# Performance work log

Measured on AMD Instinct MI355X. Metric: run time of the kernel, lower is better.

The kernel has to match this reference:

```python
import jax, jax.numpy as jnp
import numpy as np

# Matches the torch constant: 1/sqrt(2*3.14159) (NOT math.pi)
INV_SQRT_2PI = 1.0 / np.sqrt(np.float32(2.0 * 3.14159))


def density_ir_normal(x):
    return INV_SQRT_2PI * jnp.exp(-0.5 * x * x)


def setup_inputs() -> dict:
    key = jax.random.key(0)
    k1, k2, k3 = jax.random.split(key, 3)
    batch = 8388608           # 2**23 output slots
    n_events = 16777216       # 2**24 scattered events (avg 2 per slot)
    idx = jax.random.randint(k1, (n_events,), 0, batch)
    vals = jax.random.normal(k2, (n_events,), dtype=jnp.float32)
    # theta0 in (0,1) (branch prob), theta1 > 0 (scale), theta2 (loc)
    thetas = jnp.array([0.7, 1.3, 0.2], dtype=jnp.float32)
    return {"batch": batch, "idx": idx, "vals": vals, "thetas": thetas}


def reference(batch, idx, vals, thetas):
    # l_4_high = min(thetas[0], 1); l_5 = max(l_4_high, 0) -> clip(theta0, 0, 1)
    l_5_lhs_integral = jnp.clip(thetas[0], 0.0, 1.0)
    l_1_cond = 1.0 - l_5_lhs_integral
    # per-event multiplicative factor (vectorized density evaluation)
    z = (vals - thetas[2]) / thetas[1]
    factors = (1.0 - l_1_cond) * density_ir_normal(z) / thetas[1]
    # multiplicative scatter; duplicate indices multiply in (matches the
    # sequential result[idx[i]] *= factor loop, product is order-invariant)
    result = jnp.ones(batch, dtype=vals.dtype).at[idx].multiply(factors)
    return result * l_1_cond
```

## Files before the change

### kernel.cpp

```cpp
#include <hip/hip_runtime.h>
#include <climits>


#define INV_SQRT_2PI 0.39894246f
#define SLOT_BITS 14
#define SLOTS (1 << SLOT_BITS)
#define NB_MAX 512
#define NBLK 512
#define BTHREADS 1024
#define TILE 4096
#define RING 32
#define QSCALE 8192.0f
#define QMASK 0x3FFFFu
#define CMASK 0xFFFFFu

#define LDS_BAR() do {                                        \
    asm volatile("s_waitcnt lgkmcnt(0)" ::: "memory");        \
    __builtin_amdgcn_s_barrier();                             \
} while (0)

__device__ __forceinline__ long long region_idx(int blk, int b, int nbuckets,
                                                int swzmask) {
    int bb = swzmask ? ((b + blk) & swzmask) : b;
    return (long long)blk * nbuckets + bb;
}

__device__ __forceinline__ void ovf_push(uint2* ovf, int* ovf_cnt, int ovcap,
                                         unsigned gslot, unsigned q) {
    int op = atomicAdd(ovf_cnt, 1);
    if (op < ovcap) ovf[op] = make_uint2(gslot, q);
}

__global__ __launch_bounds__(BTHREADS) void bin_kernel(
        const int* __restrict__ idx, const float* __restrict__ vals,
        const float* __restrict__ thetas,
        unsigned* __restrict__ pairs,
        int* __restrict__ fill,
        uint2* __restrict__ ovf, int* __restrict__ ovf_cnt, int ovcap,
        int n, int nbuckets, int cap_shift, int swzmask, int epb) {
    __shared__ unsigned ring[RING * NB_MAX];
    __shared__ int scnt[NB_MAX];

    const int tid = threadIdx.x;
    const int blk = blockIdx.x;
    const int cappb = 1 << cap_shift;
    long long start = (long long)blk * epb;
    long long end = start + epb;
    if (end > n) end = n;

    for (int b = tid; b < nbuckets; b += BTHREADS) scnt[b] = 0;
    __syncthreads();

    const float t1 = thetas[1], t2 = thetas[2];
    const float t0c = fminf(fmaxf(thetas[0], 0.0f), 1.0f);
    const float inv_t1 = 1.0f / t1;

    int4 ck = make_int4(0,0,0,0); float4 cv = make_float4(0,0,0,0); int ccnt = 0;
    int4 pk_; float4 pv_;
    {
        long long te0 = start + TILE; if (te0 > end) te0 = end;
        long long base = start + (long long)tid * 4;
        if (base + 4 <= te0) {
            ck = *(const int4*)(idx + base);
            cv = *(const float4*)(vals + base);
            ccnt = 4;
        } else if (base < te0) {
            ccnt = (int)(te0 - base);
            int kk[4] = {0,0,0,0}; float vv[4] = {0,0,0,0};
            for (int i = 0; i < ccnt; ++i) { kk[i]=idx[base+i]; vv[i]=vals[base+i]; }
            ck = make_int4(kk[0],kk[1],kk[2],kk[3]);
            cv = make_float4(vv[0],vv[1],vv[2],vv[3]);
        }
    }

    for (long long ts = start; ts < end; ts += TILE) {
        int ncnt = 0;
        long long tsn = ts + TILE;
        if (tsn < end) {
            long long ten = tsn + TILE; if (ten > end) ten = end;
            long long base = tsn + (long long)tid * 4;
            if (base + 4 <= ten) {
                pk_ = *(const int4*)(idx + base);
                pv_ = *(const float4*)(vals + base);
                ncnt = 4;
            } else if (base < ten) {
                ncnt = (int)(ten - base);
                int kk[4] = {0,0,0,0}; float vv[4] = {0,0,0,0};
                for (int i = 0; i < ncnt; ++i) { kk[i]=idx[base+i]; vv[i]=vals[base+i]; }
                pk_ = make_int4(kk[0],kk[1],kk[2],kk[3]);
                pv_ = make_float4(vv[0],vv[1],vv[2],vv[3]);
            }
        }

        int   kk[4] = {ck.x, ck.y, ck.z, ck.w};
        float vv[4] = {cv.x, cv.y, cv.z, cv.w};
        int bs[4]; unsigned recs[4];
        #pragma unroll
        for (int j = 0; j < 4; ++j) {
            unsigned uk = (unsigned)kk[j];
            bs[j] = (int)(uk >> SLOT_BITS);
            float z = (vv[j] - t2) * inv_t1;
            float u = 0.5f * z * z;
            unsigned q = __float2uint_rn(fminf(u * QSCALE, (float)QMASK));
            recs[j] = ((uk & (SLOTS - 1)) << 18) | q;
        }
        int ret[4];
        #pragma unroll
        for (int j = 0; j < 4; ++j) {
            ret[j] = (j < ccnt && bs[j] < nbuckets)
                     ? atomicAdd(&scnt[bs[j]], 1) : INT_MIN;
        }
        #pragma unroll
        for (int j = 0; j < 4; ++j) {
            if (ret[j] == INT_MIN) continue;
            int pos = ret[j] & CMASK;
            int fl  = (ret[j] >> 20) << 4;
            if (pos - fl < RING)
                ring[(pos & (RING - 1)) * nbuckets + bs[j]] = recs[j];
            else
                ovf_push(ovf, ovf_cnt, ovcap, (unsigned)kk[j], recs[j] & QMASK);
        }
        LDS_BAR();

        for (int b = tid; b < nbuckets; b += BTHREADS) {
            int pk = scnt[b];
            int c = pk & CMASK;
            int J = pk >> 20;
            int fl = J << 4;
            int se = c < fl + RING ? c : fl + RING;
            int na = se - fl;
            int J0 = J;
            while (na >= 16) {
                int H = (J & 1) << 4;
                unsigned tmp[16];
                #pragma unroll
                for (int i = 0; i < 16; ++i)
                    tmp[i] = ring[(H + i) * nbuckets + b];
                if (J < (cappb >> 4)) {
                    uint4* d4 = (uint4*)(pairs +
                        (region_idx(blk, b, nbuckets, swzmask) << cap_shift) + (J << 4));
                    const uint4* t4 = (const uint4*)tmp;
                    d4[0]=t4[0]; d4[1]=t4[1]; d4[2]=t4[2]; d4[3]=t4[3];
                } else {
                    for (int i = 0; i < 16; ++i) {
                        unsigned r = tmp[i];
                        ovf_push(ovf, ovf_cnt, ovcap,
                                 ((unsigned)b << SLOT_BITS) | (r >> 18), r & QMASK);
                    }
                }
                ++J; fl += 16; na -= 16;
            }
            if (J != J0 || se != c) scnt[b] = (J << 20) | se;
        }
        LDS_BAR();

        ck = pk_; cv = pv_; ccnt = ncnt;
    }

    for (int b = tid; b < nbuckets; b += BTHREADS) {
        int pk = scnt[b];
        int c = pk & CMASK;
        int J = pk >> 20;
        int fl = J << 4;
        int r = c - fl;
        int valid = fl;
        if (r > 0 && J < (cappb >> 4)) {
            int H = (J & 1) << 4;
            unsigned tmp[16];
            #pragma unroll
            for (int i = 0; i < 16; ++i)
                tmp[i] = ring[(H + i) * nbuckets + b];
            uint4* d4 = (uint4*)(pairs +
                (region_idx(blk, b, nbuckets, swzmask) << cap_shift) + (J << 4));
            const uint4* t4 = (const uint4*)tmp;
            d4[0]=t4[0]; d4[1]=t4[1]; d4[2]=t4[2]; d4[3]=t4[3];
            valid = fl + r;
        } else if (r > 0) {
            int H = (J & 1) << 4;
            for (int i = 0; i < r; ++i) {
                unsigned rr = ring[(H + i) * nbuckets + b];
                ovf_push(ovf, ovf_cnt, ovcap,
                         ((unsigned)b << SLOT_BITS) | (rr >> 18), rr & QMASK);
            }
        }
        fill[region_idx(blk, b, nbuckets, swzmask)] = valid;
    }
}

__global__ __launch_bounds__(1024) void reduce_kernel(
        const unsigned* __restrict__ pairs, const int* __restrict__ fill,
        const uint2* __restrict__ ovf, const int* __restrict__ ovf_cnt, int ovcap,
        const float* __restrict__ thetas, float* __restrict__ out,
        long long n_out, int nbuckets, int cap_shift, int swzmask) {
    __shared__ unsigned accu[SLOTS];
    const int tid = threadIdx.x;
    const int b = blockIdx.x;

    for (int s = tid; s < SLOTS; s += 1024) accu[s] = 0u;
    __syncthreads();

    const int wave = tid >> 6, lane = tid & 63;
    const int SEGS = NBLK / 16;

    int sl = wave + (lane & 31) * 16;
    int cntv = fill[region_idx(sl, b, nbuckets, swzmask)];

    const unsigned* pc = pairs +
        (region_idx(wave, b, nbuckets, swzmask) << cap_shift);
    unsigned a0 = pc[lane];
    unsigned a1 = pc[64 + lane];

    for (int i = 0; i < SEGS; ++i) {
        const unsigned* pn = pc; unsigned n0 = 0, n1 = 0;
        if (i < SEGS - 1) {
            int sn = wave + (i + 1) * 16;
            pn = pairs + (region_idx(sn, b, nbuckets, swzmask) << cap_shift);
            n0 = pn[lane];
            n1 = pn[64 + lane];
        }
        int ca = __builtin_amdgcn_readlane(cntv, i);
        if (lane < ca)      atomicAdd(&accu[a0 >> 18], (1u << 25) + (a0 & QMASK));
        if (64 + lane < ca) atomicAdd(&accu[a1 >> 18], (1u << 25) + (a1 & QMASK));
        for (int r = 128 + lane; r < ca; r += 64) {
            unsigned rec = pc[r];
            atomicAdd(&accu[rec >> 18], (1u << 25) + (rec & QMASK));
        }
        pc = pn; a0 = n0; a1 = n1;
    }
    __syncthreads();

    int no = *ovf_cnt; if (no > ovcap) no = ovcap;
    for (int i = tid; i < no; i += 1024) {
        uint2 e = ovf[i];
        if ((int)(e.x >> SLOT_BITS) == b)
            atomicAdd(&accu[e.x & (SLOTS - 1)], (1u << 25) + e.y);
    }
    __syncthreads();

    const float t1 = thetas[1];
    const float t0c = fminf(fmaxf(thetas[0], 0.0f), 1.0f);
    const float logC = logf(t0c * INV_SQRT_2PI / t1);
    const float cond = 1.0f - t0c;
    long long obase = (long long)b << SLOT_BITS;
    for (int ss = tid; ss < SLOTS; ss += 1024) {
        long long o = obase + ss;
        if (o < n_out) {
            unsigned av = accu[ss];
            float v = (float)(av >> 25) * logC
                    - (float)(av & 0x1FFFFFFu) * (1.0f / QSCALE);
            out[o] = cond * expf(v);
        }
    }
}

__global__ void init_zero_kernel(float* __restrict__ out, int n) {
    int i = blockIdx.x * blockDim.x + threadIdx.x;
    int stride = gridDim.x * blockDim.x;
    for (; i < n; i += stride) out[i] = 0.0f;
}
__global__ void scatter_log_kernel(const int* __restrict__ idx,
                                   const float* __restrict__ vals,
                                   const float* __restrict__ thetas,
                                   float* __restrict__ acc, int n) {
    float t1 = thetas[1], t2 = thetas[2];
    float t0c = fminf(fmaxf(thetas[0], 0.0f), 1.0f);
    float logC = logf(t0c * INV_SQRT_2PI / t1);
    float inv_t1 = 1.0f / t1;
    int i = blockIdx.x * blockDim.x + threadIdx.x;
    int stride = gridDim.x * blockDim.x;
    for (; i < n; i += stride) {
        float z = (vals[i] - t2) * inv_t1;
        atomicAdd(&acc[idx[i]], fmaf(-0.5f * z, z, logC));
    }
}
__global__ void finalize_kernel(float* __restrict__ out,
                                const float* __restrict__ thetas, int n) {
    float t0c = fminf(fmaxf(thetas[0], 0.0f), 1.0f);
    float cond = 1.0f - t0c;
    int i = blockIdx.x * blockDim.x + threadIdx.x;
    int stride = gridDim.x * blockDim.x;
    for (; i < n; i += stride) out[i] = cond * expf(out[i]);
}

extern "C" void kernel_launch(void* const* d_in, const int* in_sizes, int n_in,
                              void* d_out, int out_size, void* d_ws, size_t ws_size,
                              hipStream_t stream) {
    const int*   idx    = (const int*)d_in[1];
    const float* vals   = (const float*)d_in[2];
    const float* thetas = (const float*)d_in[3];
    float*       out    = (float*)d_out;

    int n_events = in_sizes[1];
    long long n_out = out_size;
    int nbuckets = (int)((n_out + SLOTS - 1) >> SLOT_BITS);

    long long tiles_total = ((long long)n_events + TILE - 1) / TILE;
    long long tpb = (tiles_total + NBLK - 1) / NBLK;
    int epb = (int)(tpb * TILE);
    long long avg = nbuckets > 0 ? (epb + nbuckets - 1) / nbuckets : 1;
    long long want = avg + avg / 2 + 32;
    int cap_shift = 6;
    while ((1LL << cap_shift) < want && cap_shift < 20) ++cap_shift;
    long long cappb = 1LL << cap_shift;
    int swzmask = (nbuckets > 0 && (nbuckets & (nbuckets - 1)) == 0)
                  ? nbuckets - 1 : 0;

    size_t pairs_b = (size_t)NBLK * nbuckets * cappb * 4;
    size_t fill_b  = (size_t)NBLK * nbuckets * 4;
    size_t head    = pairs_b + fill_b + 64;
    bool fast = (nbuckets > 0) && (nbuckets <= NB_MAX) && (n_events > 0) &&
                (ws_size >= head + 64 * 1024) &&
                ((long long)NBLK * 2048  , true);

    if (fast) {
        unsigned* pairs = (unsigned*)d_ws;
        int* fill = (int*)((char*)d_ws + pairs_b);
        int* ovf_cnt = (int*)((char*)d_ws + pairs_b + fill_b);
        uint2* ovf = (uint2*)((char*)d_ws + head);
        long long ovcap_ll = (long long)((ws_size - head) / 8);
        int ovcap = (int)(ovcap_ll > 4194304 ? 4194304 : ovcap_ll);

        hipMemsetAsync(ovf_cnt, 0, sizeof(int), stream);
        bin_kernel<<<NBLK, BTHREADS, 0, stream>>>(idx, vals, thetas, pairs, fill,
                                                  ovf, ovf_cnt, ovcap,
                                                  n_events, nbuckets, cap_shift,
                                                  swzmask, epb);
        reduce_kernel<<<nbuckets, 1024, 0, stream>>>(pairs, fill, ovf, ovf_cnt,
                                                     ovcap, thetas, out,
                                                     n_out, nbuckets, cap_shift,
                                                     swzmask);
    } else {
        const int BLOCK = 256;
        int grid_out = min((int)((n_out + BLOCK - 1) / BLOCK), 2048);
        int grid_ev  = min((n_events + BLOCK - 1) / BLOCK, 2048);
        init_zero_kernel<<<grid_out, BLOCK, 0, stream>>>(out, (int)n_out);
        scatter_log_kernel<<<grid_ev, BLOCK, 0, stream>>>(idx, vals, thetas, out, n_events);
        finalize_kernel<<<grid_out, BLOCK, 0, stream>>>(out, thetas, (int)n_out);
    }
}
```

Baseline: 96.43 us.

## Double-buffer bin rings so flushing overlaps binning with one barrier per tile

```diff
diff --git a/kernel.cpp b/kernel.cpp
--- a/kernel.cpp
+++ b/kernel.cpp
@@ -3,15 +3,15 @@
 
 
 #define INV_SQRT_2PI 0.39894246f
-#define SLOT_BITS 14
+#define SLOT_BITS 15
 #define SLOTS (1 << SLOT_BITS)
-#define NB_MAX 512
+#define NB 256
 #define NBLK 512
 #define BTHREADS 1024
-#define TILE 4096
+#define TILE 2048
 #define RING 32
 #define QSCALE 8192.0f
-#define QMASK 0x3FFFFu
+#define QMASK 0x1FFFFu
 #define CMASK 0xFFFFFu
 
 #define LDS_BAR() do {                                        \
@@ -38,152 +38,170 @@
         int* __restrict__ fill,
         uint2* __restrict__ ovf, int* __restrict__ ovf_cnt, int ovcap,
         int n, int nbuckets, int cap_shift, int swzmask, int epb) {
-    __shared__ unsigned ring[RING * NB_MAX];
-    __shared__ int scnt[NB_MAX];
+    __shared__ unsigned ring[2 * RING * NB];
+    __shared__ int scnt[2 * NB];
 
     const int tid = threadIdx.x;
     const int blk = blockIdx.x;
-    const int cappb = 1 << cap_shift;
+    const int HALF = 1 << (cap_shift - 1);
+    const int HALFCH = HALF >> 4;
     long long start = (long long)blk * epb;
     long long end = start + epb;
     if (end > n) end = n;
 
-    for (int b = tid; b < nbuckets; b += BTHREADS) scnt[b] = 0;
+    for (int b = tid; b < 2 * NB; b += BTHREADS) scnt[b] = 0;
     __syncthreads();
 
     const float t1 = thetas[1], t2 = thetas[2];
     const float t0c = fminf(fmaxf(thetas[0], 0.0f), 1.0f);
     const float inv_t1 = 1.0f / t1;
 
-    int4 ck = make_int4(0,0,0,0); float4 cv = make_float4(0,0,0,0); int ccnt = 0;
-    int4 pk_; float4 pv_;
+    const bool is_flusher = (tid & 63) < 16;
+    const int fb = ((tid >> 6) << 4) + (tid & 63);
+
+    int2 ck = make_int2(0, 0); float2 cv = make_float2(0.f, 0.f); int ccnt = 0;
+    int2 pk2; float2 pv2;
     {
         long long te0 = start + TILE; if (te0 > end) te0 = end;
-        long long base = start + (long long)tid * 4;
-        if (base + 4 <= te0) {
-            ck = *(const int4*)(idx + base);
-            cv = *(const float4*)(vals + base);
-            ccnt = 4;
+        long long base = start + (long long)tid * 2;
+        if (base + 2 <= te0) {
+            ck = *(const int2*)(idx + base);
+            cv = *(const float2*)(vals + base);
+            ccnt = 2;
         } else if (base < te0) {
-            ccnt = (int)(te0 - base);
-            int kk[4] = {0,0,0,0}; float vv[4] = {0,0,0,0};
-            for (int i = 0; i < ccnt; ++i) { kk[i]=idx[base+i]; vv[i]=vals[base+i]; }
-            ck = make_int4(kk[0],kk[1],kk[2],kk[3]);
-            cv = make_float4(vv[0],vv[1],vv[2],vv[3]);
-        }
-    }
-
-    for (long long ts = start; ts < end; ts += TILE) {
+            ccnt = 1; ck.x = idx[base]; cv.x = vals[base];
+        }
+    }
+
+    int t = 0;
+    for (long long ts = start; ts < end; ts += TILE, ++t) {
+        const int p = t & 1, q = p ^ 1;
+
         int ncnt = 0;
         long long tsn = ts + TILE;
         if (tsn < end) {
             long long ten = tsn + TILE; if (ten > end) ten = end;
-            long long base = tsn + (long long)tid * 4;
-            if (base + 4 <= ten) {
-                pk_ = *(const int4*)(idx + base);
-                pv_ = *(const float4*)(vals + base);
-                ncnt = 4;
+            long long base = tsn + (long long)tid * 2;
+            if (base + 2 <= ten) {
+                pk2 = *(const int2*)(idx + base);
+                pv2 = *(const float2*)(vals + base);
+                ncnt = 2;
             } else if (base < ten) {
-                ncnt = (int)(ten - base);
-                int kk[4] = {0,0,0,0}; float vv[4] = {0,0,0,0};
-                for (int i = 0; i < ncnt; ++i) { kk[i]=idx[base+i]; vv[i]=vals[base+i]; }
-                pk_ = make_int4(kk[0],kk[1],kk[2],kk[3]);
-                pv_ = make_float4(vv[0],vv[1],vv[2],vv[3]);
+                ncnt = 1; pk2.x = idx[base]; pv2.x = vals[base];
             }
         }
 
-        int   kk[4] = {ck.x, ck.y, ck.z, ck.w};
-        float vv[4] = {cv.x, cv.y, cv.z, cv.w};
-        int bs[4]; unsigned recs[4];
+        int   kk[2] = {ck.x, ck.y};
+        float vv[2] = {cv.x, cv.y};
         #pragma unroll
-        for (int j = 0; j < 4; ++j) {
+        for (int j = 0; j < 2; ++j) {
+            if (j >= ccnt) continue;
             unsigned uk = (unsigned)kk[j];
-            bs[j] = (int)(uk >> SLOT_BITS);
+            int b = (int)(uk >> SLOT_BITS);
+            if (b >= nbuckets) continue;
             float z = (vv[j] - t2) * inv_t1;
             float u = 0.5f * z * z;
-            unsigned q = __float2uint_rn(fminf(u * QSCALE, (float)QMASK));
-            recs[j] = ((uk & (SLOTS - 1)) << 18) | q;
-        }
-        int ret[4];
-        #pragma unroll
-        for (int j = 0; j < 4; ++j) {
-            ret[j] = (j < ccnt && bs[j] < nbuckets)
-                     ? atomicAdd(&scnt[bs[j]], 1) : INT_MIN;
-        }
-        #pragma unroll
-        for (int j = 0; j < 4; ++j) {
-            if (ret[j] == INT_MIN) continue;
-            int pos = ret[j] & CMASK;
-            int fl  = (ret[j] >> 20) << 4;
+            unsigned qq = __float2uint_rn(fminf(u * QSCALE, (float)QMASK));
+            unsigned rec = ((uk & (SLOTS - 1)) << 17) | qq;
+            int ret = atomicAdd(&scnt[p * NB + b], 1);
+            int pos = ret & CMASK;
+            int fl = (ret >> 20) << 4;
             if (pos - fl < RING)
-                ring[(pos & (RING - 1)) * nbuckets + bs[j]] = recs[j];
+                ring[(p * RING + (pos & (RING - 1))) * NB + b] = rec;
             else
-                ovf_push(ovf, ovf_cnt, ovcap, (unsigned)kk[j], recs[j] & QMASK);
-        }
-        LDS_BAR();
-
-        for (int b = tid; b < nbuckets; b += BTHREADS) {
-            int pk = scnt[b];
+                ovf_push(ovf, ovf_cnt, ovcap, uk, qq);
+        }
+
+        if (is_flusher && fb < nbuckets) {
+            int pk = scnt[q * NB + fb];
             int c = pk & CMASK;
             int J = pk >> 20;
             int fl = J << 4;
             int se = c < fl + RING ? c : fl + RING;
             int na = se - fl;
-            int J0 = J;
+            bool upd = (se != c);
             while (na >= 16) {
                 int H = (J & 1) << 4;
                 unsigned tmp[16];
                 #pragma unroll
                 for (int i = 0; i < 16; ++i)
-                    tmp[i] = ring[(H + i) * nbuckets + b];
-                if (J < (cappb >> 4)) {
+                    tmp[i] = ring[(q * RING + H + i) * NB + fb];
+                if (J < HALFCH) {
                     uint4* d4 = (uint4*)(pairs +
-                        (region_idx(blk, b, nbuckets, swzmask) << cap_shift) + (J << 4));
+                        (region_idx(blk, fb, nbuckets, swzmask) << cap_shift)
+                        + q * HALF + (J << 4));
                     const uint4* t4 = (const uint4*)tmp;
                     d4[0]=t4[0]; d4[1]=t4[1]; d4[2]=t4[2]; d4[3]=t4[3];
                 } else {
-                    for (int i = 0; i < 16; ++i) {
-                        unsigned r = tmp[i];
+                    for (int i = 0; i < 16; ++i)
                         ovf_push(ovf, ovf_cnt, ovcap,
-                                 ((unsigned)b << SLOT_BITS) | (r >> 18), r & QMASK);
+                                 ((unsigned)fb << SLOT_BITS) | (tmp[i] >> 17),
+                                 tmp[i] & QMASK);
+                }
+                ++J; fl += 16; na -= 16; upd = true;
+            }
+            if (upd) scnt[q * NB + fb] = (J << 20) | se;
+        }
+
+        LDS_BAR();
+        ck = pk2; cv = pv2; ccnt = ncnt;
+    }
+
+    if (is_flusher && fb < nbuckets) {
+        int vc[2];
+        #pragma unroll
+        for (int pp = 0; pp < 2; ++pp) {
+            int pk = scnt[pp * NB + fb];
+            int c = pk & CMASK;
+            int J = pk >> 20;
+            int fl = J << 4;
+            int se = c < fl + RING ? c : fl + RING;
+            while (se - fl >= 16) {
+                unsigned tmp[16];
+                #pragma unroll
+                for (int i = 0; i < 16; ++i)
+                    tmp[i] = ring[(pp * RING + ((fl + i) & (RING - 1))) * NB + fb];
+                if (J < HALFCH) {
+                    uint4* d4 = (uint4*)(pairs +
+                        (region_idx(blk, fb, nbuckets, swzmask) << cap_shift)
+                        + pp * HALF + (J << 4));
+                    const uint4* t4 = (const uint4*)tmp;
+                    d4[0]=t4[0]; d4[1]=t4[1]; d4[2]=t4[2]; d4[3]=t4[3];
+                    ++J;
+                } else {
+                    for (int i = 0; i < 16; ++i)
+                        ovf_push(ovf, ovf_cnt, ovcap,
+                                 ((unsigned)fb << SLOT_BITS) | (tmp[i] >> 17),
+                                 tmp[i] & QMASK);
+                }
+                fl += 16;
+            }
+            int r = se - fl;
+            int rw = 0;
+            if (r > 0) {
+                if (J < HALFCH) {
+                    unsigned tmp[16];
+                    #pragma unroll
+                    for (int i = 0; i < 16; ++i)
+                        tmp[i] = ring[(pp * RING + ((fl + i) & (RING - 1))) * NB + fb];
+                    uint4* d4 = (uint4*)(pairs +
+                        (region_idx(blk, fb, nbuckets, swzmask) << cap_shift)
+                        + pp * HALF + (J << 4));
+                    const uint4* t4 = (const uint4*)tmp;
+                    d4[0]=t4[0]; d4[1]=t4[1]; d4[2]=t4[2]; d4[3]=t4[3];
+                    rw = r;
+                } else {
+                    for (int i = 0; i < r; ++i) {
+                        unsigned rr = ring[(pp * RING + ((fl + i) & (RING - 1))) * NB + fb];
+                        ovf_push(ovf, ovf_cnt, ovcap,
+                                 ((unsigned)fb << SLOT_BITS) | (rr >> 17),
+                                 rr & QMASK);
                     }
                 }
-                ++J; fl += 16; na -= 16;
             }
-            if (J != J0 || se != c) scnt[b] = (J << 20) | se;
-        }
-        LDS_BAR();
-
-        ck = pk_; cv = pv_; ccnt = ncnt;
-    }
-
-    for (int b = tid; b < nbuckets; b += BTHREADS) {
-        int pk = scnt[b];
-        int c = pk & CMASK;
-        int J = pk >> 20;
-        int fl = J << 4;
-        int r = c - fl;
-        int valid = fl;
-        if (r > 0 && J < (cappb >> 4)) {
-            int H = (J & 1) << 4;
-            unsigned tmp[16];
-            #pragma unroll
-            for (int i = 0; i < 16; ++i)
-                tmp[i] = ring[(H + i) * nbuckets + b];
-            uint4* d4 = (uint4*)(pairs +
-                (region_idx(blk, b, nbuckets, swzmask) << cap_shift) + (J << 4));
-            const uint4* t4 = (const uint4*)tmp;
-            d4[0]=t4[0]; d4[1]=t4[1]; d4[2]=t4[2]; d4[3]=t4[3];
-            valid = fl + r;
-        } else if (r > 0) {
-            int H = (J & 1) << 4;
-            for (int i = 0; i < r; ++i) {
-                unsigned rr = ring[(H + i) * nbuckets + b];
-                ovf_push(ovf, ovf_cnt, ovcap,
-                         ((unsigned)b << SLOT_BITS) | (rr >> 18), rr & QMASK);
-            }
-        }
-        fill[region_idx(blk, b, nbuckets, swzmask)] = valid;
+            vc[pp] = (J << 4) + rw;
+        }
+        fill[region_idx(blk, fb, nbuckets, swzmask)] = (vc[1] << 8) | vc[0];
     }
 }
 
@@ -191,7 +209,7 @@
         const unsigned* __restrict__ pairs, const int* __restrict__ fill,
         const uint2* __restrict__ ovf, const int* __restrict__ ovf_cnt, int ovcap,
         const float* __restrict__ thetas, float* __restrict__ out,
-        long long n_out, int nbuckets, int cap_shift, int swzmask) {
+        long long n_out, int nbuckets, int swzmask) {
     __shared__ unsigned accu[SLOTS];
     const int tid = threadIdx.x;
     const int b = blockIdx.x;
@@ -205,27 +223,26 @@
     int sl = wave + (lane & 31) * 16;
     int cntv = fill[region_idx(sl, b, nbuckets, swzmask)];
 
-    const unsigned* pc = pairs +
-        (region_idx(wave, b, nbuckets, swzmask) << cap_shift);
-    unsigned a0 = pc[lane];
-    unsigned a1 = pc[64 + lane];
+    const unsigned* pc = pairs + (region_idx(wave, b, nbuckets, swzmask) << 8);
+    unsigned a0 = pc[lane], a1 = pc[64 + lane];
+    unsigned a2 = pc[128 + lane], a3 = pc[192 + lane];
 
     for (int i = 0; i < SEGS; ++i) {
-        const unsigned* pn = pc; unsigned n0 = 0, n1 = 0;
+        unsigned n0 = 0, n1 = 0, n2 = 0, n3 = 0;
         if (i < SEGS - 1) {
             int sn = wave + (i + 1) * 16;
-            pn = pairs + (region_idx(sn, b, nbuckets, swzmask) << cap_shift);
-            n0 = pn[lane];
-            n1 = pn[64 + lane];
-        }
-        int ca = __builtin_amdgcn_readlane(cntv, i);
-        if (lane < ca)      atomicAdd(&accu[a0 >> 18], (1u << 25) + (a0 & QMASK));
-        if (64 + lane < ca) atomicAdd(&accu[a1 >> 18], (1u << 25) + (a1 & QMASK));
-        for (int r = 128 + lane; r < ca; r += 64) {
-            unsigned rec = pc[r];
-            atomicAdd(&accu[rec >> 18], (1u << 25) + (rec & QMASK));
-        }
-        pc = pn; a0 = n0; a1 = n1;
+            const unsigned* pn = pairs +
+                (region_idx(sn, b, nbuckets, swzmask) << 8);
+            n0 = pn[lane]; n1 = pn[64 + lane];
+            n2 = pn[128 + lane]; n3 = pn[192 + lane];
+        }
+        int cpk = __builtin_amdgcn_readlane(cntv, i);
+        int cA = cpk & 0xFF, cB = (cpk >> 8) & 0xFF;
+        if (lane < cA)      atomicAdd(&accu[a0 >> 17], (1u << 25) + (a0 & QMASK));
+        if (64 + lane < cA) atomicAdd(&accu[a1 >> 17], (1u << 25) + (a1 & QMASK));
+        if (lane < cB)      atomicAdd(&accu[a2 >> 17], (1u << 25) + (a2 & QMASK));
+        if (64 + lane < cB) atomicAdd(&accu[a3 >> 17], (1u << 25) + (a3 & QMASK));
+        a0 = n0; a1 = n1; a2 = n2; a3 = n3;
     }
     __syncthreads();
 
@@ -298,7 +315,7 @@
     long long tpb = (tiles_total + NBLK - 1) / NBLK;
     int epb = (int)(tpb * TILE);
     long long avg = nbuckets > 0 ? (epb + nbuckets - 1) / nbuckets : 1;
-    long long want = avg + avg / 2 + 32;
+    long long want = avg + avg / 2 + 64;
     int cap_shift = 6;
     while ((1LL << cap_shift) < want && cap_shift < 20) ++cap_shift;
     long long cappb = 1LL << cap_shift;
@@ -308,9 +325,8 @@
     size_t pairs_b = (size_t)NBLK * nbuckets * cappb * 4;
     size_t fill_b  = (size_t)NBLK * nbuckets * 4;
     size_t head    = pairs_b + fill_b + 64;
-    bool fast = (nbuckets > 0) && (nbuckets <= NB_MAX) && (n_events > 0) &&
-                (ws_size >= head + 64 * 1024) &&
-                ((long long)NBLK * 2048  , true);
+    bool fast = (nbuckets > 0) && (nbuckets <= NB) && (n_events > 0) &&
+                (cap_shift == 8) && (ws_size >= head + 64 * 1024);
 
     if (fast) {
         unsigned* pairs = (unsigned*)d_ws;
@@ -327,8 +343,7 @@
                                                   swzmask, epb);
         reduce_kernel<<<nbuckets, 1024, 0, stream>>>(pairs, fill, ovf, ovf_cnt,
                                                      ovcap, thetas, out,
-                                                     n_out, nbuckets, cap_shift,
-                                                     swzmask);
+                                                     n_out, nbuckets, swzmask);
     } else {
         const int BLOCK = 256;
         int grid_out = min((int)((n_out + BLOCK - 1) / BLOCK), 2048);
```

Result: slower. 103.3 us (+7.1%).
